# Kernel optimization log

Measured on AMD Instinct MI355X. Metric: run time of the kernel, lower is better.

Reference implementation:

```python
import jax, jax.numpy as jnp
import numpy as np

B, T, V, U = 128, 256, 256, 2048


def setup_inputs() -> dict:
    key = jax.random.key(0)
    k_x, k_wx, k_wh, k_wd = jax.random.split(key, 4)
    x = jax.random.randint(k_x, (B, T), 0, V)
    # glorot-ish scaling so tanh doesn't saturate
    Wx = jax.random.normal(k_wx, (V, U), jnp.float32) * (1.0 / np.sqrt(V))
    Wh = jax.random.normal(k_wh, (U, U), jnp.float32) * (1.0 / np.sqrt(U))
    b = jnp.zeros((U,), jnp.float32)
    Wd = jax.random.normal(k_wd, (U, V), jnp.float32) * (1.0 / np.sqrt(U))
    bd = jnp.zeros((V,), jnp.float32)
    h0 = jnp.zeros((B, U), jnp.float32)
    return {"x": x, "Wx": Wx, "Wh": Wh, "b": b, "Wd": Wd, "bd": bd, "h0": h0}


def reference(x, Wx, Wh, b, Wd, bd, h0):
    # one_hot(x, V) @ Wx  ==  Wx[x]  (row gather; avoids materializing one-hot)
    x_proj = Wx[x] + b  # [B, T, U]
    x_proj_t = jnp.swapaxes(x_proj, 0, 1)  # [T, B, U] for scan

    def step(h, xt):
        # SimpleRNN cell: h_t = tanh(x_t Wx + h_{t-1} Wh + b)
        h_new = jnp.tanh(xt + h @ Wh)
        return h_new, h_new

    _, hs = jax.lax.scan(step, h0, x_proj_t)  # hs: [T, B, U]
    hs = jnp.swapaxes(hs, 0, 1)  # [B, T, U]
    logits = jnp.einsum('btu,uv->btv', hs, Wd) + bd  # [B, T, V]
    return logits
```

## Files before the change

kernel.cpp:

```cpp
#include <hip/hip_runtime.h>
#include <hip/hip_bf16.h>

#define B_ 128
#define T_ 256
#define V_ 256
#define U_ 2048

typedef __bf16 bf16x8 __attribute__((ext_vector_type(8)));
typedef float f32x4 __attribute__((ext_vector_type(4)));

union B8u { uint4 u; bf16x8 v; };

static __device__ inline bf16x8 u2b(uint4 u) { B8u t; t.u = u; return t.v; }
static __device__ inline bf16x8 ldg8(const unsigned short* p) {
    B8u t; t.u = *reinterpret_cast<const uint4*>(p); return t.v;
}
static __device__ inline bf16x8 lds8(const char* smem, unsigned off) {
    B8u t; t.u = *reinterpret_cast<const uint4*>(smem + off); return t.v;
}
static __device__ inline unsigned short f2b(float f) {
    __hip_bfloat16 h = __float2bfloat16(f);
    unsigned short r; __builtin_memcpy(&r, &h, 2); return r;
}
static __device__ inline uint4 ldg16_c(const unsigned short* p) {
    uint4 r;
    asm volatile("global_load_dwordx4 %0, %1, off"
                 : "=&v"(r) : "v"(p) : "memory");
    return r;
}
static __device__ inline void stg2_sc(unsigned short* p, unsigned short v) {
    unsigned vv = v;
    asm volatile("global_store_short %0, %1, off sc0 sc1"
                 :: "v"(p), "v"(vv) : "memory");
}


__global__ void transpose_bf16(const float* __restrict__ in,
                               unsigned short* __restrict__ outp, int R, int C) {
    __shared__ float tile[32][33];
    int tc = blockIdx.x * 32, tr = blockIdx.y * 32;
    int lx = threadIdx.x & 31, ly = threadIdx.x >> 5;
#pragma unroll
    for (int i = 0; i < 32; i += 8)
        tile[ly + i][lx] = in[(size_t)(tr + ly + i) * C + tc + lx];
    __syncthreads();
#pragma unroll
    for (int i = 0; i < 32; i += 8)
        outp[(size_t)(tc + ly + i) * R + tr + lx] = f2b(tile[lx][ly + i]);
}

__global__ void conv_h0(const float* __restrict__ h0, unsigned short* __restrict__ hb) {
    int i = blockIdx.x * blockDim.x + threadIdx.x;
    hb[i] = f2b(h0[i]);
}

__global__ void transpose_x(const int* __restrict__ x, int* __restrict__ xT) {
    int i = blockIdx.x * 256 + threadIdx.x;
    int b = i >> 8, t = i & 255;
    xT[t * B_ + b] = x[i];
}

__global__ __launch_bounds__(256, 1) void rnn_arc2(
        const int* __restrict__ xT, const float* __restrict__ Wx,
        const float* __restrict__ bias, const unsigned short* __restrict__ WhT,
        unsigned short* __restrict__ hs, unsigned* __restrict__ ctrs) {
    extern __shared__ char smem[];
    float* red = (float*)(smem + 32 * 2048 * 2);

    const int bid = blockIdx.x;
    const int g = bid >> 6, p = bid & 63;
    const int b0 = g * 32, c0 = p * 32;
    const int tid = threadIdx.x;
    const int w = tid >> 6, lane = tid & 63;
    const int lr = lane & 15, lh = lane >> 4;
    const int mi = w >> 1, ni = w & 1;

    for (int i = tid; i < 32 * 256; i += 256) {
        int c = i >> 8, k8 = i & 255;
        uint4 v = *reinterpret_cast<const uint4*>(WhT + (size_t)(c0 + c) * U_ + k8 * 8);
        unsigned off = (unsigned)(c * 4096 + k8 * 16) ^ ((unsigned)(c & 7) << 4);
        *reinterpret_cast<uint4*>(smem + off) = v;
    }
    __syncthreads();

    const int kbase = w * 512;
    const unsigned lin0 = (unsigned)(lr * 4096) + (unsigned)((kbase + lh * 8) * 2);
    const unsigned lin1 = lin0 + 16 * 4096;
    const unsigned swz = (unsigned)(lr & 7) << 4;

    const int erow = mi * 16 + lh * 4;
    const int ucol = c0 + ni * 16 + lr;
    const float bs = bias[ucol];
    const int redbase = (mi * 16 + lh * 4) * 34 + ni * 16 + lr;

    float xp[4];
#pragma unroll
    for (int r = 0; r < 4; ++r) {
        int tok = xT[0 * B_ + b0 + erow + r];
        xp[r] = Wx[(size_t)tok * U_ + ucol] + bs;
    }

    for (int t = 0; t < T_; ++t) {
        const unsigned short* hp = hs + (size_t)t * (B_ * U_);
        unsigned short* hc = hs + (size_t)(t + 1) * (B_ * U_);

        const unsigned short* pa0 = hp + (size_t)(b0 + lr) * U_ + kbase + lh * 8;
        const unsigned short* pa1 = pa0 + 16 * U_;
        uint4 areg0[16], areg1[16];
#pragma unroll
        for (int ks = 0; ks < 16; ++ks) {
            areg0[ks] = ldg16_c(pa0 + ks * 32);
            areg1[ks] = ldg16_c(pa1 + ks * 32);
        }
        asm volatile("s_waitcnt vmcnt(0)" ::: "memory");
        __builtin_amdgcn_sched_barrier(0);

        f32x4 acc00 = {0.f, 0.f, 0.f, 0.f}, acc01 = {0.f, 0.f, 0.f, 0.f};
        f32x4 acc10 = {0.f, 0.f, 0.f, 0.f}, acc11 = {0.f, 0.f, 0.f, 0.f};
#pragma unroll
        for (int ks = 0; ks < 16; ++ks) {
            bf16x8 a0 = u2b(areg0[ks]);
            bf16x8 a1 = u2b(areg1[ks]);
            bf16x8 bb0 = lds8(smem, (lin0 + (unsigned)ks * 64u) ^ swz);
            bf16x8 bb1 = lds8(smem, (lin1 + (unsigned)ks * 64u) ^ swz);
            acc00 = __builtin_amdgcn_mfma_f32_16x16x32_bf16(a0, bb0, acc00, 0, 0, 0);
            acc01 = __builtin_amdgcn_mfma_f32_16x16x32_bf16(a0, bb1, acc01, 0, 0, 0);
            acc10 = __builtin_amdgcn_mfma_f32_16x16x32_bf16(a1, bb0, acc10, 0, 0, 0);
            acc11 = __builtin_amdgcn_mfma_f32_16x16x32_bf16(a1, bb1, acc11, 0, 0, 0);
        }

        float* redw = red + w * (32 * 34);
#pragma unroll
        for (int r = 0; r < 4; ++r) {
            redw[(lh * 4 + r) * 34 + lr] = acc00[r];
            redw[(lh * 4 + r) * 34 + 16 + lr] = acc01[r];
            redw[(16 + lh * 4 + r) * 34 + lr] = acc10[r];
            redw[(16 + lh * 4 + r) * 34 + 16 + lr] = acc11[r];
        }
        __syncthreads();

#pragma unroll
        for (int r = 0; r < 4; ++r) {
            int o = redbase + r * 34;
            float z = red[0 * 1088 + o] + red[1 * 1088 + o] +
                      red[2 * 1088 + o] + red[3 * 1088 + o];
            float hv = tanhf(z + xp[r]);
            stg2_sc(hc + (size_t)(b0 + erow + r) * U_ + ucol, f2b(hv));
        }

        if (t + 1 < T_) {
#pragma unroll
            for (int r = 0; r < 4; ++r) {
                int tok = xT[(t + 1) * B_ + b0 + erow + r];
                xp[r] = Wx[(size_t)tok * U_ + ucol] + bs;
            }
        }

        asm volatile("s_waitcnt vmcnt(0)" ::: "memory");
        __syncthreads();
        if (tid == 0)
            __hip_atomic_fetch_add(ctrs + (g * 8 + (p & 7)) * 32, 1u,
                                   __ATOMIC_RELAXED, __HIP_MEMORY_SCOPE_AGENT);

        if (w == 0) {
            unsigned tgt = (unsigned)(t + 1) * 8u;
            unsigned* cp = ctrs + (g * 8 + (lane & 7)) * 32;
            while (__hip_atomic_load(cp, __ATOMIC_RELAXED, __HIP_MEMORY_SCOPE_AGENT) < tgt)
                __builtin_amdgcn_s_sleep(1);
        }
        __syncthreads();
    }
}

__global__ __launch_bounds__(256, 1) void decode_gemm(
        const unsigned short* __restrict__ hsD, const unsigned short* __restrict__ WdT,
        const float* __restrict__ bdv, float* __restrict__ out) {
    const int tid = threadIdx.x;
    const int w = tid >> 6, lane = tid & 63;
    const int lr = lane & 15, lh = lane >> 4;
    const int r0 = blockIdx.x * 128 + w * 32;

    const unsigned short* pa0 = hsD + (size_t)(r0 + lr) * U_ + lh * 8;
    const unsigned short* pa1 = pa0 + (size_t)16 * U_;
    const unsigned short* pb = WdT + (size_t)lr * U_ + lh * 8;

    f32x4 acc0[16], acc1[16];
#pragma unroll
    for (int n = 0; n < 16; ++n) {
        acc0[n] = (f32x4){0.f, 0.f, 0.f, 0.f};
        acc1[n] = (f32x4){0.f, 0.f, 0.f, 0.f};
    }

    for (int ks = 0; ks < 64; ++ks) {
        bf16x8 a0 = ldg8(pa0 + ks * 32);
        bf16x8 a1 = ldg8(pa1 + ks * 32);
#pragma unroll
        for (int n = 0; n < 16; ++n) {
            bf16x8 bb = ldg8(pb + (size_t)n * 16 * U_ + ks * 32);
            acc0[n] = __builtin_amdgcn_mfma_f32_16x16x32_bf16(a0, bb, acc0[n], 0, 0, 0);
            acc1[n] = __builtin_amdgcn_mfma_f32_16x16x32_bf16(a1, bb, acc1[n], 0, 0, 0);
        }
    }

#pragma unroll
    for (int n = 0; n < 16; ++n) {
        float bd_ = bdv[n * 16 + lr];
#pragma unroll
        for (int r = 0; r < 4; ++r) {
            int m0 = r0 + lh * 4 + r;
            int m1 = m0 + 16;
            out[((size_t)(m0 & 127) * T_ + (m0 >> 7)) * V_ + n * 16 + lr] = acc0[n][r] + bd_;
            out[((size_t)(m1 & 127) * T_ + (m1 >> 7)) * V_ + n * 16 + lr] = acc1[n][r] + bd_;
        }
    }
}

extern "C" void kernel_launch(void* const* d_in, const int* in_sizes, int n_in,
                              void* d_out, int out_size, void* d_ws, size_t ws_size,
                              hipStream_t stream) {
    const int* x = (const int*)d_in[0];
    const float* Wx = (const float*)d_in[1];
    const float* Wh = (const float*)d_in[2];
    const float* b = (const float*)d_in[3];
    const float* Wd = (const float*)d_in[4];
    const float* bd = (const float*)d_in[5];
    const float* h0 = (const float*)d_in[6];
    float* out = (float*)d_out;

    char* ws = (char*)d_ws;

    const size_t OFF_WhT = 0;
    const size_t OFF_WdT = 8388608;
    const size_t OFF_xT = 9437184;
    const size_t OFF_CTR = 9568256;
    const size_t OFF_HS = 9572352;

    unsigned short* WhT = (unsigned short*)(ws + OFF_WhT);
    unsigned short* WdT = (unsigned short*)(ws + OFF_WdT);
    int* xT = (int*)(ws + OFF_xT);
    unsigned* ctrs = (unsigned*)(ws + OFF_CTR);
    unsigned short* hs = (unsigned short*)(ws + OFF_HS);

    hipMemsetAsync(ctrs, 0, 4096, stream);
    transpose_bf16<<<dim3(64, 64), 256, 0, stream>>>(Wh, WhT, 2048, 2048);
    transpose_bf16<<<dim3(8, 64), 256, 0, stream>>>(Wd, WdT, 2048, 256);
    conv_h0<<<1024, 256, 0, stream>>>(h0, hs);
    transpose_x<<<128, 256, 0, stream>>>(x, xT);

    const int smem_bytes = 32 * 2048 * 2 + 4 * 32 * 34 * 4;
    hipFuncSetAttribute((const void*)rnn_arc2, hipFuncAttributeMaxDynamicSharedMemorySize,
                        smem_bytes);
    void* args[] = {(void*)&xT, (void*)&Wx, (void*)&b, (void*)&WhT, (void*)&hs,
                    (void*)&ctrs};
    hipLaunchCooperativeKernel((const void*)rnn_arc2, dim3(256), dim3(256), args,
                               (unsigned)smem_bytes, stream);

    const unsigned short* hsD = hs + (size_t)B_ * U_;
    decode_gemm<<<256, 256, 0, stream>>>(hsD, WdT, bd, out);
}
```

Baseline: 1.935 ms.

## Move per-step barrier wait to loop top, split load wait, vectorize epilogue stores

The per-step grid wait moves from the end of the step to the start of the next one. Each wave now polls only the two counters covering the k-range it will read, spinning without sleep, which removes a block-wide __syncthreads and the s_sleep from the critical path. Counters are now indexed by column group (p>>3), so a wave waits only on its producers. The h-load wait is split into two halves so MFMAs can start on the first half while the rest is still in flight. The epilogue is reorganised so each thread handles 4 contiguous columns, with vectorized LDS reads and 8-byte stores, and the reduction buffer is padded to stride 36. The risks are heavier polling traffic and subtle memory-ordering correctness.

```diff
diff --git a/kernel.cpp b/kernel.cpp
--- a/kernel.cpp
+++ b/kernel.cpp
@@ -28,10 +28,9 @@
                  : "=&v"(r) : "v"(p) : "memory");
     return r;
 }
-static __device__ inline void stg2_sc(unsigned short* p, unsigned short v) {
-    unsigned vv = v;
-    asm volatile("global_store_short %0, %1, off sc0 sc1"
-                 :: "v"(p), "v"(vv) : "memory");
+static __device__ inline void stg8_sc(unsigned short* p, uint2 v) {
+    asm volatile("global_store_dwordx2 %0, %1, off sc0 sc1"
+                 :: "v"(p), "v"(v) : "memory");
 }
 
 
@@ -60,7 +59,7 @@
     xT[t * B_ + b] = x[i];
 }
 
-__global__ __launch_bounds__(256, 1) void rnn_arc2(
+__global__ __launch_bounds__(256, 1) void rnn_arc3(
         const int* __restrict__ xT, const float* __restrict__ Wx,
         const float* __restrict__ bias, const unsigned short* __restrict__ WhT,
         unsigned short* __restrict__ hs, unsigned* __restrict__ ctrs) {
@@ -73,7 +72,6 @@
     const int tid = threadIdx.x;
     const int w = tid >> 6, lane = tid & 63;
     const int lr = lane & 15, lh = lane >> 4;
-    const int mi = w >> 1, ni = w & 1;
 
     for (int i = tid; i < 32 * 256; i += 256) {
         int c = i >> 8, k8 = i & 255;
@@ -88,22 +86,27 @@
     const unsigned lin1 = lin0 + 16 * 4096;
     const unsigned swz = (unsigned)(lr & 7) << 4;
 
-    const int erow = mi * 16 + lh * 4;
-    const int ucol = c0 + ni * 16 + lr;
-    const float bs = bias[ucol];
-    const int redbase = (mi * 16 + lh * 4) * 34 + ni * 16 + lr;
-
-    float xp[4];
-#pragma unroll
-    for (int r = 0; r < 4; ++r) {
-        int tok = xT[0 * B_ + b0 + erow + r];
-        xp[r] = Wx[(size_t)tok * U_ + ucol] + bs;
+    const int erow = tid >> 3;
+    const int ec4 = (tid & 7) * 4;
+    const int ucol = c0 + ec4;
+    const f32x4 bias4 = *reinterpret_cast<const f32x4*>(bias + ucol);
+
+    f32x4 xp;
+    {
+        int tok = xT[0 * B_ + b0 + erow];
+        xp = *reinterpret_cast<const f32x4*>(Wx + (size_t)tok * U_ + ucol) + bias4;
     }
 
     for (int t = 0; t < T_; ++t) {
         const unsigned short* hp = hs + (size_t)t * (B_ * U_);
         unsigned short* hc = hs + (size_t)(t + 1) * (B_ * U_);
 
+        if (t > 0 && lane < 2) {
+            unsigned tgt = (unsigned)t * 8u;
+            unsigned* cp = ctrs + (g * 8 + (w * 2 + lane)) * 32;
+            while (__hip_atomic_load(cp, __ATOMIC_RELAXED, __HIP_MEMORY_SCOPE_AGENT) < tgt) {}
+        }
+
         const unsigned short* pa0 = hp + (size_t)(b0 + lr) * U_ + kbase + lh * 8;
         const unsigned short* pa1 = pa0 + 16 * U_;
         uint4 areg0[16], areg1[16];
@@ -112,13 +115,14 @@
             areg0[ks] = ldg16_c(pa0 + ks * 32);
             areg1[ks] = ldg16_c(pa1 + ks * 32);
         }
-        asm volatile("s_waitcnt vmcnt(0)" ::: "memory");
-        __builtin_amdgcn_sched_barrier(0);
 
         f32x4 acc00 = {0.f, 0.f, 0.f, 0.f}, acc01 = {0.f, 0.f, 0.f, 0.f};
         f32x4 acc10 = {0.f, 0.f, 0.f, 0.f}, acc11 = {0.f, 0.f, 0.f, 0.f};
-#pragma unroll
-        for (int ks = 0; ks < 16; ++ks) {
+
+        asm volatile("s_waitcnt vmcnt(16)" ::: "memory");
+        __builtin_amdgcn_sched_barrier(0);
+#pragma unroll
+        for (int ks = 0; ks < 8; ++ks) {
             bf16x8 a0 = u2b(areg0[ks]);
             bf16x8 a1 = u2b(areg1[ks]);
             bf16x8 bb0 = lds8(smem, (lin0 + (unsigned)ks * 64u) ^ swz);
@@ -128,47 +132,52 @@
             acc10 = __builtin_amdgcn_mfma_f32_16x16x32_bf16(a1, bb0, acc10, 0, 0, 0);
             acc11 = __builtin_amdgcn_mfma_f32_16x16x32_bf16(a1, bb1, acc11, 0, 0, 0);
         }
-
-        float* redw = red + w * (32 * 34);
+        asm volatile("s_waitcnt vmcnt(0)" ::: "memory");
+        __builtin_amdgcn_sched_barrier(0);
+#pragma unroll
+        for (int ks = 8; ks < 16; ++ks) {
+            bf16x8 a0 = u2b(areg0[ks]);
+            bf16x8 a1 = u2b(areg1[ks]);
+            bf16x8 bb0 = lds8(smem, (lin0 + (unsigned)ks * 64u) ^ swz);
+            bf16x8 bb1 = lds8(smem, (lin1 + (unsigned)ks * 64u) ^ swz);
+            acc00 = __builtin_amdgcn_mfma_f32_16x16x32_bf16(a0, bb0, acc00, 0, 0, 0);
+            acc01 = __builtin_amdgcn_mfma_f32_16x16x32_bf16(a0, bb1, acc01, 0, 0, 0);
+            acc10 = __builtin_amdgcn_mfma_f32_16x16x32_bf16(a1, bb0, acc10, 0, 0, 0);
+            acc11 = __builtin_amdgcn_mfma_f32_16x16x32_bf16(a1, bb1, acc11, 0, 0, 0);
+        }
+
+        float* redw = red + w * 1152;
 #pragma unroll
         for (int r = 0; r < 4; ++r) {
-            redw[(lh * 4 + r) * 34 + lr] = acc00[r];
-            redw[(lh * 4 + r) * 34 + 16 + lr] = acc01[r];
-            redw[(16 + lh * 4 + r) * 34 + lr] = acc10[r];
-            redw[(16 + lh * 4 + r) * 34 + 16 + lr] = acc11[r];
+            redw[(lh * 4 + r) * 36 + lr] = acc00[r];
+            redw[(lh * 4 + r) * 36 + 16 + lr] = acc01[r];
+            redw[(16 + lh * 4 + r) * 36 + lr] = acc10[r];
+            redw[(16 + lh * 4 + r) * 36 + 16 + lr] = acc11[r];
         }
         __syncthreads();
 
-#pragma unroll
-        for (int r = 0; r < 4; ++r) {
-            int o = redbase + r * 34;
-            float z = red[0 * 1088 + o] + red[1 * 1088 + o] +
-                      red[2 * 1088 + o] + red[3 * 1088 + o];
-            float hv = tanhf(z + xp[r]);
-            stg2_sc(hc + (size_t)(b0 + erow + r) * U_ + ucol, f2b(hv));
+        {
+            const int o = erow * 36 + ec4;
+            f32x4 z = *reinterpret_cast<f32x4*>(red + 0 * 1152 + o);
+            z += *reinterpret_cast<f32x4*>(red + 1 * 1152 + o);
+            z += *reinterpret_cast<f32x4*>(red + 2 * 1152 + o);
+            z += *reinterpret_cast<f32x4*>(red + 3 * 1152 + o);
+            z += xp;
+            unsigned lo = (unsigned)f2b(tanhf(z[0])) | ((unsigned)f2b(tanhf(z[1])) << 16);
+            unsigned hi = (unsigned)f2b(tanhf(z[2])) | ((unsigned)f2b(tanhf(z[3])) << 16);
+            stg8_sc(hc + (size_t)(b0 + erow) * U_ + ucol, make_uint2(lo, hi));
         }
 
         if (t + 1 < T_) {
-#pragma unroll
-            for (int r = 0; r < 4; ++r) {
-                int tok = xT[(t + 1) * B_ + b0 + erow + r];
-                xp[r] = Wx[(size_t)tok * U_ + ucol] + bs;
-            }
+            int tok = xT[(t + 1) * B_ + b0 + erow];
+            xp = *reinterpret_cast<const f32x4*>(Wx + (size_t)tok * U_ + ucol) + bias4;
         }
 
         asm volatile("s_waitcnt vmcnt(0)" ::: "memory");
         __syncthreads();
         if (tid == 0)
-            __hip_atomic_fetch_add(ctrs + (g * 8 + (p & 7)) * 32, 1u,
+            __hip_atomic_fetch_add(ctrs + (g * 8 + (p >> 3)) * 32, 1u,
                                    __ATOMIC_RELAXED, __HIP_MEMORY_SCOPE_AGENT);
-
-        if (w == 0) {
-            unsigned tgt = (unsigned)(t + 1) * 8u;
-            unsigned* cp = ctrs + (g * 8 + (lane & 7)) * 32;
-            while (__hip_atomic_load(cp, __ATOMIC_RELAXED, __HIP_MEMORY_SCOPE_AGENT) < tgt)
-                __builtin_amdgcn_s_sleep(1);
-        }
-        __syncthreads();
     }
 }
 
@@ -247,12 +256,12 @@
     conv_h0<<<1024, 256, 0, stream>>>(h0, hs);
     transpose_x<<<128, 256, 0, stream>>>(x, xT);
 
-    const int smem_bytes = 32 * 2048 * 2 + 4 * 32 * 34 * 4;
-    hipFuncSetAttribute((const void*)rnn_arc2, hipFuncAttributeMaxDynamicSharedMemorySize,
+    const int smem_bytes = 32 * 2048 * 2 + 4 * 1152 * 4;
+    hipFuncSetAttribute((const void*)rnn_arc3, hipFuncAttributeMaxDynamicSharedMemorySize,
                         smem_bytes);
     void* args[] = {(void*)&xT, (void*)&Wx, (void*)&b, (void*)&WhT, (void*)&hs,
                     (void*)&ctrs};
-    hipLaunchCooperativeKernel((const void*)rnn_arc2, dim3(256), dim3(256), args,
+    hipLaunchCooperativeKernel((const void*)rnn_arc3, dim3(256), dim3(256), args,
                                (unsigned)smem_bytes, stream);
 
     const unsigned short* hsD = hs + (size_t)B_ * U_;
```

Measured after the change: 2.008 ms. 3.8% more time.
